# Kernel tuning notes

Hardware: AMD Instinct MI355X
Metric: run time of the kernel (lower is better)

The kernel has to match this reference:

```python
import jax, jax.numpy as jnp
import numpy as np

N_NODES = 50000
N_EDGES = 600000
D = 128
LN_EPS = 1e-5


def _mlp_ln(x, W1, b1, W2, b2, g, beta):
    # Linear -> ReLU -> Linear -> LayerNorm (standard MeshGraphNets model_fn)
    h = jax.nn.relu(x @ W1 + b1)
    y = h @ W2 + b2
    mu = jnp.mean(y, axis=-1, keepdims=True)
    var = jnp.var(y, axis=-1, keepdims=True)
    return (y - mu) * jax.lax.rsqrt(var + LN_EPS) * g + beta


def setup_inputs() -> dict:
    key = jax.random.key(0)
    ks = jax.random.split(key, 16)
    def glorot(k, shape):
        fan = shape[0] + shape[1]
        return jax.random.normal(k, shape, jnp.float32) * np.sqrt(2.0 / fan)
    inp = {
        "node_features": jax.random.normal(ks[0], (1, N_NODES, D), jnp.float32),
        "edge_features": jax.random.normal(ks[1], (1, N_EDGES, D), jnp.float32),
        "senders": jax.random.randint(ks[2], (N_EDGES,), 0, N_NODES),
        "receivers": jax.random.randint(ks[3], (N_EDGES,), 0, N_NODES),
        # edge MLP: in 3*D -> 128 -> D, LayerNorm
        "eW1": glorot(ks[4], (3 * D, 128)), "eb1": jnp.zeros((128,), jnp.float32),
        "eW2": glorot(ks[5], (128, D)), "eb2": jnp.zeros((D,), jnp.float32),
        "eg": jnp.ones((D,), jnp.float32), "ebeta": jnp.zeros((D,), jnp.float32),
        # node MLP: in 2*D -> 128 -> D, LayerNorm
        "nW1": glorot(ks[6], (2 * D, 128)), "nb1": jnp.zeros((128,), jnp.float32),
        "nW2": glorot(ks[7], (128, D)), "nb2": jnp.zeros((D,), jnp.float32),
        "ng": jnp.ones((D,), jnp.float32), "nbeta": jnp.zeros((D,), jnp.float32),
        # attention linear D -> 1
        "aW": glorot(ks[8], (D, 1)), "ab": jnp.zeros((1,), jnp.float32),
    }
    return inp


def reference(node_features, edge_features, senders, receivers,
              eW1, eb1, eW2, eb2, eg, ebeta,
              nW1, nb1, nW2, nb2, ng, nbeta,
              aW, ab):
    # --- edge update: gather + concat + MLP ---
    sf = node_features[:, senders]      # [1,E,D]
    rf = node_features[:, receivers]    # [1,E,D]
    new_ef = _mlp_ln(jnp.concatenate([sf, rf, edge_features], -1),
                     eW1, eb1, eW2, eb2, eg, ebeta)  # [1,E,D]
    # --- per-edge attention: linear + LeakyReLU + scatter_softmax over receivers ---
    logits = jax.nn.leaky_relu(new_ef @ aW + ab, 0.2)[0, :, 0]  # [E]
    seg_max = jax.ops.segment_max(logits, receivers, num_segments=N_NODES)
    seg_max = jnp.where(jnp.isfinite(seg_max), seg_max, 0.0)
    ex = jnp.exp(logits - seg_max[receivers])
    seg_sum = jax.ops.segment_sum(ex, receivers, num_segments=N_NODES)
    att = ex / seg_sum[receivers]  # [E]
    # --- scatter-add aggregation ---
    agg = jax.ops.segment_sum(new_ef[0] * att[:, None], receivers,
                              num_segments=N_NODES)[None]  # [1,N,D]
    new_nf = _mlp_ln(jnp.concatenate([node_features, agg], -1),
                     nW1, nb1, nW2, nb2, ng, nbeta)  # [1,N,D]
    # residual connections
    new_nf = new_nf + node_features
    new_ef = new_ef + edge_features
    return new_nf, new_ef
```

## Files before the change

kernel.cpp:

```cpp
#include <hip/hip_runtime.h>
#include <hip/hip_bf16.h>

#define N_NODES 50000
#define N_EDGES 600000
#define D 128
#define LN_EPS 1e-5f

typedef float f32x4 __attribute__((ext_vector_type(4)));
typedef int   i32x4 __attribute__((ext_vector_type(4)));
typedef short s16x8 __attribute__((ext_vector_type(8)));

#define W1P_OFF     0u
#define W2P_OFF     98304u
#define NW1P_OFF    131072u
#define NW2P_OFF    196608u
#define DEG_OFF     229376u
#define ROWPTR_OFF  429440u
#define LOGITS_OFF  629504u
#define CURSOR_OFF  3029504u
#define ELIST_OFF   3229504u
#define AGG_OFF     5629504u
#define RAW_OFF     31229504u
#define WS_NEED_RAW (RAW_OFF + (size_t)N_EDGES * D * 2)

static __device__ __forceinline__ unsigned short f2bf(float f) {
    unsigned int u = __float_as_uint(f);
    u = (u + 0x7FFFu + ((u >> 16) & 1u)) >> 16;
    return (unsigned short)u;
}
static __device__ __forceinline__ float bf2f(unsigned short h) {
    return __uint_as_float(((unsigned int)h) << 16);
}
static __device__ __forceinline__ int pkbf2(float a, float b) {
    union { __hip_bfloat16 h[2]; int i; } u;
    u.h[0] = __float2bfloat16(a);
    u.h[1] = __float2bfloat16(b);
    return u.i;
}
union frag_u { i32x4 i; s16x8 s; };
static __device__ __forceinline__ f32x4 mfma_bf16(s16x8 a, s16x8 b, f32x4 c) {
    return __builtin_amdgcn_mfma_f32_16x16x32_bf16(a, b, c, 0, 0, 0);
}

__global__ void k_init(const float* __restrict__ eW1, const float* __restrict__ eW2,
                       const float* __restrict__ nW1, const float* __restrict__ nW2,
                       char* __restrict__ ws) {
    int idx = blockIdx.x * 256 + threadIdx.x;
    if (idx < N_NODES) {
        ((int*)(ws + DEG_OFF))[idx] = 0;
        ((int*)(ws + CURSOR_OFF))[idx] = 0;
    }
    int e = idx & 7, lane = (idx >> 3) & 63, ct = (idx >> 9) & 7, ks = idx >> 12;
    int k = ks * 32 + (lane >> 4) * 8 + e;
    int j = ct * 16 + (lane & 15);
    if (idx < 12 * 4096) ((unsigned short*)(ws + W1P_OFF))[idx]  = f2bf(eW1[k * 128 + j]);
    if (idx < 4 * 4096)  ((unsigned short*)(ws + W2P_OFF))[idx]  = f2bf(eW2[k * 128 + j]);
    if (idx < 8 * 4096)  ((unsigned short*)(ws + NW1P_OFF))[idx] = f2bf(nW1[k * 128 + j]);
    if (idx < 4 * 4096)  ((unsigned short*)(ws + NW2P_OFF))[idx] = f2bf(nW2[k * 128 + j]);
}

__global__ void k_count(const int* __restrict__ rcv, int* __restrict__ deg) {
    int e = blockIdx.x * 256 + threadIdx.x;
    if (e < N_EDGES) atomicAdd(&deg[rcv[e]], 1);
}

__global__ void k_scan(const int* __restrict__ deg, int* __restrict__ rowptr) {
    __shared__ int part[256];
    const int tid = threadIdx.x;
    const int CH = (N_NODES + 255) / 256;
    const int base = tid * CH;
    int s = 0;
    for (int i = 0; i < CH; ++i) { int idx = base + i; if (idx < N_NODES) s += deg[idx]; }
    part[tid] = s;
    __syncthreads();
    if (tid == 0) {
        int run = 0;
        for (int j = 0; j < 256; ++j) { int t = part[j]; part[j] = run; run += t; }
        rowptr[N_NODES] = run;
    }
    __syncthreads();
    int run = part[tid];
    for (int i = 0; i < CH; ++i) {
        int idx = base + i;
        if (idx < N_NODES) { rowptr[idx] = run; run += deg[idx]; }
    }
}

__global__ void k_fill(const int* __restrict__ rcv, const int* __restrict__ rowptr,
                       int* __restrict__ cursor, int* __restrict__ elist) {
    int e = blockIdx.x * 256 + threadIdx.x;
    if (e >= N_EDGES) return;
    int r = rcv[e];
    int slot = atomicAdd(&cursor[r], 1);
    elist[rowptr[r] + slot] = e;
}

template <int STORE_RAW>
__global__ __launch_bounds__(256, 4) void k_edge(
    const float* __restrict__ nf, const float* __restrict__ ef,
    const int* __restrict__ snd, const int* __restrict__ rcv,
    const i32x4* __restrict__ B1, const i32x4* __restrict__ B2,
    const float* __restrict__ b1, const float* __restrict__ b2,
    const float* __restrict__ g, const float* __restrict__ beta,
    const float* __restrict__ aW, const float* __restrict__ ab,
    float* __restrict__ out_ef, float* __restrict__ logits,
    unsigned short* __restrict__ rawbuf)
{
    __shared__ __align__(16) char  hbuf[64 * 128 * 2];
    __shared__ __align__(16) i32x4 bstage[2][512];
    const int tid = threadIdx.x, lane = tid & 63, rt = tid >> 6;
    const int j0 = lane & 15, hi = lane >> 4;

    const long eA = (long)blockIdx.x * 64 + rt * 16 + j0;
    const int sA = snd[eA], rA = rcv[eA];
    const float* __restrict__ prowS = nf + (size_t)sA * D;
    const float* __restrict__ prowR = nf + (size_t)rA * D;
    const float* __restrict__ prowE = ef + (size_t)eA * D;

    {
        i32x4 p0 = B1[tid], p1 = B1[256 + tid];
        bstage[0][tid]       = p0;
        bstage[0][256 + tid] = p1;
    }
    i32x4 t0 = B1[512 + tid], t1 = B1[768 + tid];
    float4 f0 = *(const float4*)(prowS + hi * 8);
    float4 f1 = *(const float4*)(prowS + hi * 8 + 4);
    __syncthreads();

    f32x4 acc[8];
    #pragma unroll
    for (int ct = 0; ct < 8; ++ct) acc[ct] = (f32x4){0.f, 0.f, 0.f, 0.f};
    for (int s = 0; s < 12; ++s) {
        const int cur = s & 1, nxt = cur ^ 1;
        bstage[nxt][tid]       = t0;
        bstage[nxt][256 + tid] = t1;
        frag_u a;
        a.i[0] = pkbf2(f0.x, f0.y); a.i[1] = pkbf2(f0.z, f0.w);
        a.i[2] = pkbf2(f1.x, f1.y); a.i[3] = pkbf2(f1.z, f1.w);
        {
            const i32x4* src = (s + 2 < 12) ? (B1 + (s + 2) * 512) : (B2 + (s + 2 - 12) * 512);
            t0 = src[tid];
            t1 = src[256 + tid];
        }
        if (s < 11) {
            const int sn = s + 1;
            const float* p = (sn < 4 ? prowS : (sn < 8 ? prowR : prowE)) + (sn & 3) * 32 + hi * 8;
            f0 = *(const float4*)p;
            f1 = *(const float4*)(p + 4);
        }
        #pragma unroll
        for (int ct = 0; ct < 8; ++ct) {
            frag_u b; b.i = bstage[cur][ct * 64 + lane];
            acc[ct] = mfma_bf16(a.s, b.s, acc[ct]);
        }
        __syncthreads();
    }

    #pragma unroll
    for (int ct = 0; ct < 8; ++ct) {
        float bb = b1[ct * 16 + j0];
        #pragma unroll
        for (int rg = 0; rg < 4; ++rg) {
            int row = rt * 16 + hi * 4 + rg;
            float y = fmaxf(acc[ct][rg] + bb, 0.0f);
            int addr = (row * 256 + (ct * 16 + j0) * 2) ^ ((row & 7) << 4);
            *(__hip_bfloat16*)(hbuf + addr) = __float2bfloat16(y);
        }
    }
    asm volatile("" ::: "memory");

    #pragma unroll
    for (int ct = 0; ct < 8; ++ct) acc[ct] = (f32x4){0.f, 0.f, 0.f, 0.f};
    {
        const int arow = rt * 16 + j0;
        for (int s2 = 0; s2 < 4; ++s2) {
            const int cur = s2 & 1, nxt = cur ^ 1;
            if (s2 < 3) {
                bstage[nxt][tid]       = t0;
                bstage[nxt][256 + tid] = t1;
            }
            if (s2 < 2) {
                const i32x4* src = B2 + (s2 + 2) * 512;
                t0 = src[tid];
                t1 = src[256 + tid];
            }
            int addr = (arow * 256 + (s2 * 32 + hi * 8) * 2) ^ ((arow & 7) << 4);
            frag_u a;
            a.i = *(const i32x4*)(hbuf + addr);
            #pragma unroll
            for (int ct = 0; ct < 8; ++ct) {
                frag_u b; b.i = bstage[cur][ct * 64 + lane];
                acc[ct] = mfma_bf16(a.s, b.s, acc[ct]);
            }
            if (s2 < 3) __syncthreads();
        }
    }

    float b2v[8], gv[8], bv[8], awv[8];
    #pragma unroll
    for (int ct = 0; ct < 8; ++ct) {
        int c = ct * 16 + j0;
        b2v[ct] = b2[c]; gv[ct] = g[c]; bv[ct] = beta[c]; awv[ct] = aW[c];
    }
    float abv = ab[0];
    #pragma unroll
    for (int rg = 0; rg < 4; ++rg) {
        int row = rt * 16 + hi * 4 + rg;
        long e = (long)blockIdx.x * 64 + row;
        float y[8]; float s = 0.f, sq = 0.f;
        #pragma unroll
        for (int ct = 0; ct < 8; ++ct) {
            y[ct] = acc[ct][rg] + b2v[ct];
            s += y[ct]; sq += y[ct] * y[ct];
        }
        #pragma unroll
        for (int m = 1; m <= 8; m <<= 1) { s += __shfl_xor(s, m); sq += __shfl_xor(sq, m); }
        float mu = s * (1.0f / 128.0f);
        float var = sq * (1.0f / 128.0f) - mu * mu;
        float rs = rsqrtf(var + LN_EPS);
        const float* efr = ef + (size_t)e * D;
        float* outr = out_ef + (size_t)e * D;
        unsigned short* rawr = STORE_RAW ? (rawbuf + (size_t)e * D) : nullptr;
        float lg = 0.f;
        #pragma unroll
        for (int ct = 0; ct < 8; ++ct) {
            int c = ct * 16 + j0;
            float o = (y[ct] - mu) * rs * gv[ct] + bv[ct];
            outr[c] = o + efr[c];
            if (STORE_RAW) rawr[c] = f2bf(o);
            lg += o * awv[ct];
        }
        #pragma unroll
        for (int m = 1; m <= 8; m <<= 1) lg += __shfl_xor(lg, m);
        if (j0 == 0) {
            float L = lg + abv;
            L = (L >= 0.f) ? L : 0.2f * L;
            logits[e] = L;
        }
    }
}

template <int USE_RAW>
__global__ __launch_bounds__(256) void k_agg(
    const int* __restrict__ rowptr, const int* __restrict__ elist,
    const float* __restrict__ logits, const unsigned int* __restrict__ raw32,
    const float* __restrict__ out_ef, const float* __restrict__ ef,
    float* __restrict__ agg)
{
    const int tid = threadIdx.x, lane = tid & 63, w = tid >> 6;
    const int r = blockIdx.x * 4 + w;
    const int beg = rowptr[r], end = rowptr[r + 1];

    float mx = -3.4e38f;
    for (int cb = beg; cb < end; cb += 64) {
        int i = cb + lane;
        float lg = (i < end) ? logits[elist[i]] : -3.4e38f;
        mx = fmaxf(mx, lg);
    }
    #pragma unroll
    for (int m = 1; m <= 32; m <<= 1) mx = fmaxf(mx, __shfl_xor(mx, m));

    float ssum = 0.f, ax = 0.f, ay = 0.f;
    for (int cb = beg; cb < end; cb += 64) {
        int i = cb + lane;
        int cnt = min(64, end - cb);
        int e = (i < end) ? elist[i] : 0;
        float wt = (i < end) ? __expf(logits[e] - mx) : 0.f;
        ssum += wt;
        for (int j = 0; j < cnt; ++j) {
            int   ej = __shfl(e, j);
            float wj = __shfl(wt, j);
            if (USE_RAW) {
                unsigned int u = raw32[(size_t)ej * 64 + lane];
                ax += bf2f((unsigned short)(u & 0xffffu)) * wj;
                ay += bf2f((unsigned short)(u >> 16)) * wj;
            } else {
                float2 o = ((const float2*)out_ef)[(size_t)ej * 64 + lane];
                float2 f = ((const float2*)ef)[(size_t)ej * 64 + lane];
                ax += (o.x - f.x) * wj;
                ay += (o.y - f.y) * wj;
            }
        }
    }
    #pragma unroll
    for (int m = 1; m <= 32; m <<= 1) ssum += __shfl_xor(ssum, m);
    float inv = (ssum > 0.f) ? 1.0f / ssum : 0.0f;
    ((float2*)agg)[(size_t)r * 64 + lane] = make_float2(ax * inv, ay * inv);
}

__global__ __launch_bounds__(256, 4) void k_node(
    const float* __restrict__ nf, const float* __restrict__ agg,
    const s16x8* __restrict__ B1, const s16x8* __restrict__ B2,
    const float* __restrict__ b1, const float* __restrict__ b2,
    const float* __restrict__ g, const float* __restrict__ beta,
    float* __restrict__ out_nf)
{
    __shared__ __align__(16) char hbuf[64 * 128 * 2];
    const int tid = threadIdx.x, lane = tid & 63, rt = tid >> 6;
    const int j0 = lane & 15, hi = lane >> 4;

    long nA = (long)blockIdx.x * 64 + rt * 16 + j0;
    if (nA >= N_NODES) nA = 0;
    const float* __restrict__ prowN = nf  + (size_t)nA * D;
    const float* __restrict__ prowA = agg + (size_t)nA * D;

    f32x4 acc[8];
    #pragma unroll
    for (int ct = 0; ct < 8; ++ct) acc[ct] = (f32x4){0.f, 0.f, 0.f, 0.f};
    #pragma unroll
    for (int ks = 0; ks < 8; ++ks) {
        const float* p = (ks < 4 ? prowN : prowA) + (ks & 3) * 32 + hi * 8;
        float4 f0 = *(const float4*)p;
        float4 f1 = *(const float4*)(p + 4);
        frag_u a;
        a.i[0] = pkbf2(f0.x, f0.y); a.i[1] = pkbf2(f0.z, f0.w);
        a.i[2] = pkbf2(f1.x, f1.y); a.i[3] = pkbf2(f1.z, f1.w);
        #pragma unroll
        for (int ct = 0; ct < 8; ++ct)
            acc[ct] = mfma_bf16(a.s, B1[(ks * 8 + ct) * 64 + lane], acc[ct]);
    }

    #pragma unroll
    for (int ct = 0; ct < 8; ++ct) {
        float bb = b1[ct * 16 + j0];
        #pragma unroll
        for (int rg = 0; rg < 4; ++rg) {
            int row = rt * 16 + hi * 4 + rg;
            float y = fmaxf(acc[ct][rg] + bb, 0.0f);
            int addr = (row * 256 + (ct * 16 + j0) * 2) ^ ((row & 7) << 4);
            *(__hip_bfloat16*)(hbuf + addr) = __float2bfloat16(y);
        }
    }
    asm volatile("" ::: "memory");

    #pragma unroll
    for (int ct = 0; ct < 8; ++ct) acc[ct] = (f32x4){0.f, 0.f, 0.f, 0.f};
    {
        int arow = rt * 16 + j0;
        #pragma unroll
        for (int ks = 0; ks < 4; ++ks) {
            int addr = (arow * 256 + (ks * 32 + hi * 8) * 2) ^ ((arow & 7) << 4);
            frag_u a;
            a.i = *(const i32x4*)(hbuf + addr);
            #pragma unroll
            for (int ct = 0; ct < 8; ++ct)
                acc[ct] = mfma_bf16(a.s, B2[(ks * 8 + ct) * 64 + lane], acc[ct]);
        }
    }

    float b2v[8], gv[8], bv[8];
    #pragma unroll
    for (int ct = 0; ct < 8; ++ct) {
        int c = ct * 16 + j0;
        b2v[ct] = b2[c]; gv[ct] = g[c]; bv[ct] = beta[c];
    }
    #pragma unroll
    for (int rg = 0; rg < 4; ++rg) {
        int row = rt * 16 + hi * 4 + rg;
        long n = (long)blockIdx.x * 64 + row;
        float y[8]; float s = 0.f, sq = 0.f;
        #pragma unroll
        for (int ct = 0; ct < 8; ++ct) {
            y[ct] = acc[ct][rg] + b2v[ct];
            s += y[ct]; sq += y[ct] * y[ct];
        }
        #pragma unroll
        for (int m = 1; m <= 8; m <<= 1) { s += __shfl_xor(s, m); sq += __shfl_xor(sq, m); }
        float mu = s * (1.0f / 128.0f);
        float var = sq * (1.0f / 128.0f) - mu * mu;
        float rs = rsqrtf(var + LN_EPS);
        if (n < N_NODES) {
            const float* nfr = nf + (size_t)n * D;
            float* outr = out_nf + (size_t)n * D;
            #pragma unroll
            for (int ct = 0; ct < 8; ++ct) {
                int c = ct * 16 + j0;
                float o = (y[ct] - mu) * rs * gv[ct] + bv[ct];
                outr[c] = o + nfr[c];
            }
        }
    }
}

extern "C" void kernel_launch(void* const* d_in, const int* in_sizes, int n_in,
                              void* d_out, int out_size, void* d_ws, size_t ws_size,
                              hipStream_t stream)
{
    (void)in_sizes; (void)n_in; (void)out_size;
    const float* nf    = (const float*)d_in[0];
    const float* ef    = (const float*)d_in[1];
    const int*   snd   = (const int*)d_in[2];
    const int*   rcv   = (const int*)d_in[3];
    const float* eW1   = (const float*)d_in[4];
    const float* eb1   = (const float*)d_in[5];
    const float* eW2   = (const float*)d_in[6];
    const float* eb2   = (const float*)d_in[7];
    const float* eg    = (const float*)d_in[8];
    const float* ebeta = (const float*)d_in[9];
    const float* nW1   = (const float*)d_in[10];
    const float* nb1   = (const float*)d_in[11];
    const float* nW2   = (const float*)d_in[12];
    const float* nb2   = (const float*)d_in[13];
    const float* ng    = (const float*)d_in[14];
    const float* nbeta = (const float*)d_in[15];
    const float* aW    = (const float*)d_in[16];
    const float* ab    = (const float*)d_in[17];

    float* out_nf = (float*)d_out;
    float* out_ef = out_nf + (size_t)N_NODES * D;
    char*  ws     = (char*)d_ws;

    const bool use_raw = (ws_size >= WS_NEED_RAW);

    k_init<<<196, 256, 0, stream>>>(eW1, eW2, nW1, nW2, ws);

    k_count<<<(N_EDGES + 255) / 256, 256, 0, stream>>>(rcv, (int*)(ws + DEG_OFF));
    k_scan<<<1, 256, 0, stream>>>((const int*)(ws + DEG_OFF), (int*)(ws + ROWPTR_OFF));
    k_fill<<<(N_EDGES + 255) / 256, 256, 0, stream>>>(
        rcv, (const int*)(ws + ROWPTR_OFF), (int*)(ws + CURSOR_OFF), (int*)(ws + ELIST_OFF));

    if (use_raw) {
        k_edge<1><<<N_EDGES / 64, 256, 0, stream>>>(
            nf, ef, snd, rcv,
            (const i32x4*)(ws + W1P_OFF), (const i32x4*)(ws + W2P_OFF),
            eb1, eb2, eg, ebeta, aW, ab,
            out_ef, (float*)(ws + LOGITS_OFF), (unsigned short*)(ws + RAW_OFF));
        k_agg<1><<<N_NODES / 4, 256, 0, stream>>>(
            (const int*)(ws + ROWPTR_OFF), (const int*)(ws + ELIST_OFF),
            (const float*)(ws + LOGITS_OFF), (const unsigned int*)(ws + RAW_OFF),
            nullptr, nullptr, (float*)(ws + AGG_OFF));
    } else {
        k_edge<0><<<N_EDGES / 64, 256, 0, stream>>>(
            nf, ef, snd, rcv,
            (const i32x4*)(ws + W1P_OFF), (const i32x4*)(ws + W2P_OFF),
            eb1, eb2, eg, ebeta, aW, ab,
            out_ef, (float*)(ws + LOGITS_OFF), nullptr);
        k_agg<0><<<N_NODES / 4, 256, 0, stream>>>(
            (const int*)(ws + ROWPTR_OFF), (const int*)(ws + ELIST_OFF),
            (const float*)(ws + LOGITS_OFF), nullptr,
            out_ef, ef, (float*)(ws + AGG_OFF));
    }

    k_node<<<(N_NODES + 63) / 64, 256, 0, stream>>>(
        nf, (const float*)(ws + AGG_OFF),
        (const s16x8*)(ws + NW1P_OFF), (const s16x8*)(ws + NW2P_OFF),
        nb1, nb2, ng, nbeta, out_nf);
}
```

Baseline: 584.1 us.

## Process 128 edges per 512-thread block in edge MLP kernel

```diff
diff --git a/kernel.cpp b/kernel.cpp
--- a/kernel.cpp
+++ b/kernel.cpp
@@ -96,7 +96,7 @@
 }
 
 template <int STORE_RAW>
-__global__ __launch_bounds__(256, 4) void k_edge(
+__global__ __launch_bounds__(512, 2) void k_edge(
     const float* __restrict__ nf, const float* __restrict__ ef,
     const int* __restrict__ snd, const int* __restrict__ rcv,
     const i32x4* __restrict__ B1, const i32x4* __restrict__ B2,
@@ -106,23 +106,21 @@
     float* __restrict__ out_ef, float* __restrict__ logits,
     unsigned short* __restrict__ rawbuf)
 {
-    __shared__ __align__(16) char  hbuf[64 * 128 * 2];
+    __shared__ __align__(16) char  hbuf[128 * 256];
     __shared__ __align__(16) i32x4 bstage[2][512];
-    const int tid = threadIdx.x, lane = tid & 63, rt = tid >> 6;
+    const int tid = threadIdx.x, lane = tid & 63, w = tid >> 6;
     const int j0 = lane & 15, hi = lane >> 4;
 
-    const long eA = (long)blockIdx.x * 64 + rt * 16 + j0;
-    const int sA = snd[eA], rA = rcv[eA];
+    const long ebase = (long)blockIdx.x * 128;
+    const long eA = ebase + w * 16 + j0;
+    const long eAc = (eA < N_EDGES) ? eA : (N_EDGES - 1);
+    const int sA = snd[eAc], rA = rcv[eAc];
     const float* __restrict__ prowS = nf + (size_t)sA * D;
     const float* __restrict__ prowR = nf + (size_t)rA * D;
-    const float* __restrict__ prowE = ef + (size_t)eA * D;
-
-    {
-        i32x4 p0 = B1[tid], p1 = B1[256 + tid];
-        bstage[0][tid]       = p0;
-        bstage[0][256 + tid] = p1;
-    }
-    i32x4 t0 = B1[512 + tid], t1 = B1[768 + tid];
+    const float* __restrict__ prowE = ef + (size_t)eAc * D;
+
+    bstage[0][tid] = B1[tid];
+    i32x4 t0 = B1[512 + tid];
     float4 f0 = *(const float4*)(prowS + hi * 8);
     float4 f1 = *(const float4*)(prowS + hi * 8 + 4);
     __syncthreads();
@@ -132,15 +130,13 @@
     for (int ct = 0; ct < 8; ++ct) acc[ct] = (f32x4){0.f, 0.f, 0.f, 0.f};
     for (int s = 0; s < 12; ++s) {
         const int cur = s & 1, nxt = cur ^ 1;
-        bstage[nxt][tid]       = t0;
-        bstage[nxt][256 + tid] = t1;
+        bstage[nxt][tid] = t0;
         frag_u a;
         a.i[0] = pkbf2(f0.x, f0.y); a.i[1] = pkbf2(f0.z, f0.w);
         a.i[2] = pkbf2(f1.x, f1.y); a.i[3] = pkbf2(f1.z, f1.w);
         {
             const i32x4* src = (s + 2 < 12) ? (B1 + (s + 2) * 512) : (B2 + (s + 2 - 12) * 512);
             t0 = src[tid];
-            t1 = src[256 + tid];
         }
         if (s < 11) {
             const int sn = s + 1;
@@ -161,7 +157,7 @@
         float bb = b1[ct * 16 + j0];
         #pragma unroll
         for (int rg = 0; rg < 4; ++rg) {
-            int row = rt * 16 + hi * 4 + rg;
+            int row = w * 16 + hi * 4 + rg;
             float y = fmaxf(acc[ct][rg] + bb, 0.0f);
             int addr = (row * 256 + (ct * 16 + j0) * 2) ^ ((row & 7) << 4);
             *(__hip_bfloat16*)(hbuf + addr) = __float2bfloat16(y);
@@ -172,18 +168,11 @@
     #pragma unroll
     for (int ct = 0; ct < 8; ++ct) acc[ct] = (f32x4){0.f, 0.f, 0.f, 0.f};
     {
-        const int arow = rt * 16 + j0;
+        const int arow = w * 16 + j0;
         for (int s2 = 0; s2 < 4; ++s2) {
             const int cur = s2 & 1, nxt = cur ^ 1;
-            if (s2 < 3) {
-                bstage[nxt][tid]       = t0;
-                bstage[nxt][256 + tid] = t1;
-            }
-            if (s2 < 2) {
-                const i32x4* src = B2 + (s2 + 2) * 512;
-                t0 = src[tid];
-                t1 = src[256 + tid];
-            }
+            if (s2 < 3) bstage[nxt][tid] = t0;
+            if (s2 < 2) t0 = B2[(s2 + 2) * 512 + tid];
             int addr = (arow * 256 + (s2 * 32 + hi * 8) * 2) ^ ((arow & 7) << 4);
             frag_u a;
             a.i = *(const i32x4*)(hbuf + addr);
@@ -205,8 +194,8 @@
     float abv = ab[0];
     #pragma unroll
     for (int rg = 0; rg < 4; ++rg) {
-        int row = rt * 16 + hi * 4 + rg;
-        long e = (long)blockIdx.x * 64 + row;
+        int row = w * 16 + hi * 4 + rg;
+        long e = ebase + row;
         float y[8]; float s = 0.f, sq = 0.f;
         #pragma unroll
         for (int ct = 0; ct < 8; ++ct) {
@@ -218,21 +207,23 @@
         float mu = s * (1.0f / 128.0f);
         float var = sq * (1.0f / 128.0f) - mu * mu;
         float rs = rsqrtf(var + LN_EPS);
-        const float* efr = ef + (size_t)e * D;
-        float* outr = out_ef + (size_t)e * D;
-        unsigned short* rawr = STORE_RAW ? (rawbuf + (size_t)e * D) : nullptr;
         float lg = 0.f;
-        #pragma unroll
-        for (int ct = 0; ct < 8; ++ct) {
-            int c = ct * 16 + j0;
-            float o = (y[ct] - mu) * rs * gv[ct] + bv[ct];
-            outr[c] = o + efr[c];
-            if (STORE_RAW) rawr[c] = f2bf(o);
-            lg += o * awv[ct];
+        if (e < N_EDGES) {
+            const float* efr = ef + (size_t)e * D;
+            float* outr = out_ef + (size_t)e * D;
+            unsigned short* rawr = STORE_RAW ? (rawbuf + (size_t)e * D) : nullptr;
+            #pragma unroll
+            for (int ct = 0; ct < 8; ++ct) {
+                int c = ct * 16 + j0;
+                float o = (y[ct] - mu) * rs * gv[ct] + bv[ct];
+                outr[c] = o + efr[c];
+                if (STORE_RAW) rawr[c] = f2bf(o);
+                lg += o * awv[ct];
+            }
         }
         #pragma unroll
         for (int m = 1; m <= 8; m <<= 1) lg += __shfl_xor(lg, m);
-        if (j0 == 0) {
+        if (j0 == 0 && e < N_EDGES) {
             float L = lg + abv;
             L = (L >= 0.f) ? L : 0.2f * L;
             logits[e] = L;
@@ -419,8 +410,9 @@
     k_fill<<<(N_EDGES + 255) / 256, 256, 0, stream>>>(
         rcv, (const int*)(ws + ROWPTR_OFF), (int*)(ws + CURSOR_OFF), (int*)(ws + ELIST_OFF));
 
+    const int edge_grid = (N_EDGES + 127) / 128;
     if (use_raw) {
-        k_edge<1><<<N_EDGES / 64, 256, 0, stream>>>(
+        k_edge<1><<<edge_grid, 512, 0, stream>>>(
             nf, ef, snd, rcv,
             (const i32x4*)(ws + W1P_OFF), (const i32x4*)(ws + W2P_OFF),
             eb1, eb2, eg, ebeta, aW, ab,
@@ -430,7 +422,7 @@
             (const float*)(ws + LOGITS_OFF), (const unsigned int*)(ws + RAW_OFF),
             nullptr, nullptr, (float*)(ws + AGG_OFF));
     } else {
-        k_edge<0><<<N_EDGES / 64, 256, 0, stream>>>(
+        k_edge<0><<<edge_grid, 512, 0, stream>>>(
             nf, ef, snd, rcv,
             (const i32x4*)(ws + W1P_OFF), (const i32x4*)(ws + W2P_OFF),
             eb1, eb2, eg, ebeta, aW, ab,
```

Result: slower. 616.7 us (+5.6%).
